# Kernel optimization log

Hardware: AMD Instinct MI355X
Metric: run time of the kernel (lower is better)

## Reference

```python
import jax, jax.numpy as jnp
import numpy as np

B, N, D, L = 8, 2048, 256, 4
LN_EPS = 1e-5


def setup_inputs() -> dict:
    key = jax.random.key(0)
    ks = jax.random.split(key, 12)
    s = 1.0 / np.sqrt(D)  # keep relu-attention scores well-scaled
    return {
        "x": jax.random.normal(ks[0], (B, N, D), jnp.float32),
        "wpe": jax.random.normal(ks[1], (N, D), jnp.float32) * 0.02,
        "Wq": jax.random.normal(ks[2], (L, D, D), jnp.float32) * s,
        "Wk": jax.random.normal(ks[3], (L, D, D), jnp.float32) * s,
        "Wv": jax.random.normal(ks[4], (L, D, D), jnp.float32) * s,
        "ln1_g": jnp.ones((L, D), jnp.float32),
        "ln1_b": jnp.zeros((L, D), jnp.float32),
        "mlp_W1": jax.random.normal(ks[5], (L, D, D), jnp.float32) * s,
        "mlp_b1": jnp.zeros((L, D), jnp.float32),
        "mlp_W2": jax.random.normal(ks[6], (L, D, D), jnp.float32) * s,
        "mlp_b2": jnp.zeros((L, D), jnp.float32),
        "ln2_g": jnp.ones((L, D), jnp.float32),
        "ln2_b": jnp.zeros((L, D), jnp.float32),
    }


def _layernorm(h, g, b):
    mu = jnp.mean(h, axis=-1, keepdims=True)
    var = jnp.mean(jnp.square(h - mu), axis=-1, keepdims=True)
    return (h - mu) * jax.lax.rsqrt(var + LN_EPS) * g + b


def reference(x, wpe, Wq, Wk, Wv, ln1_g, ln1_b, mlp_W1, mlp_b1, mlp_W2, mlp_b2, ln2_g, ln2_b):
    n = x.shape[1]
    # causal averaging mask: mask[i,j] = 1/(i+1) if j <= i else 0
    idx = jnp.arange(n)
    mask = (idx[None, :] <= idx[:, None]).astype(x.dtype) / (idx[:, None] + 1).astype(x.dtype)
    H = x + wpe[:n][None, :, :]  # positional embedding (position_ids = arange)
    for l in range(L):
        q = jnp.einsum('bnd,de->bne', H, Wq[l])
        k = jnp.einsum('bnd,de->bne', H, Wk[l])
        v = jnp.einsum('bnd,de->bne', H, Wv[l])
        attn = jax.nn.relu(jnp.einsum('bid,bjd->bij', q, k)) * mask[None, :, :]
        H = H + jnp.einsum('bij,bjd->bid', attn, v)
        H = _layernorm(H, ln1_g[l], ln1_b[l])
        h1 = jax.nn.relu(jnp.einsum('bnd,de->bne', H, mlp_W1[l]) + mlp_b1[l])
        H = H + jnp.einsum('bnd,de->bne', h1, mlp_W2[l]) + mlp_b2[l]
        H = _layernorm(H, ln2_g[l], ln2_b[l])
    return H
```

## Files before the change

kernel.cpp:

```cpp
#include <hip/hip_runtime.h>

#define Dd 256
#define Nn 2048
#define Bb 8
#define Ll 4
#define Mm (Bb*Nn)

typedef __attribute__((ext_vector_type(8))) short short8;
typedef __attribute__((ext_vector_type(4))) float f32x4;
typedef unsigned short u16;

__device__ __forceinline__ u16 f2bf(float f) {
  unsigned int u = __float_as_uint(f);
  u = (u + 0x7FFFu + ((u >> 16) & 1u)) >> 16;
  return (u16)u;
}
__device__ __forceinline__ float bf2f(u16 h) {
  return __uint_as_float(((unsigned int)h) << 16);
}
__device__ __forceinline__ void split2(float v, u16& hi, u16& lo) {
  hi = f2bf(v);
  lo = f2bf(v - bf2f(hi));
}

__global__ void prep_w3(const float* __restrict__ Wq, const float* __restrict__ Wk,
                        const float* __restrict__ Wv, const float* __restrict__ W1,
                        const float* __restrict__ W2,
                        u16* __restrict__ qh, u16* __restrict__ ql,
                        u16* __restrict__ kh, u16* __restrict__ kl,
                        u16* __restrict__ vh, u16* __restrict__ vl,
                        u16* __restrict__ w1h, u16* __restrict__ w1l,
                        u16* __restrict__ w2h, u16* __restrict__ w2l) {
  int idx = blockIdx.x * 256 + threadIdx.x;
  int l = idx >> 16, rem = idx & 65535;
  int e = rem >> 8, d = rem & 255;
  int src = (l << 16) | (d << 8) | e;
  u16 h, lo;
  split2(Wq[src], h, lo); qh[idx] = h;  ql[idx] = lo;
  split2(Wk[src], h, lo); kh[idx] = h;  kl[idx] = lo;
  split2(Wv[src], h, lo); vh[idx] = h;  vl[idx] = lo;
  split2(W1[src], h, lo); w1h[idx] = h; w1l[idx] = lo;
  split2(W2[src], h, lo); w2h[idx] = h; w2l[idx] = lo;
}

__global__ void add_pe3(const float* __restrict__ x, const float* __restrict__ wpe,
                        float* __restrict__ H, u16* __restrict__ Hh, u16* __restrict__ Hl) {
  int idx = blockIdx.x * 256 + threadIdx.x;
  int nd = (idx << 2) & (Nn * Dd - 1);
  float4 xv = ((const float4*)x)[idx];
  float4 pv = *(const float4*)(wpe + nd);
  float4 h;
  h.x = xv.x + pv.x; h.y = xv.y + pv.y; h.z = xv.z + pv.z; h.w = xv.w + pv.w;
  ((float4*)H)[idx] = h;
  ushort4 hv, lv;
  split2(h.x, hv.x, lv.x); split2(h.y, hv.y, lv.y);
  split2(h.z, hv.z, lv.z); split2(h.w, hv.w, lv.w);
  ((ushort4*)Hh)[idx] = hv;
  ((ushort4*)Hl)[idx] = lv;
}

__global__ __launch_bounds__(256) void ln3(const float* __restrict__ Hin,
      float* __restrict__ Hout, u16* __restrict__ Hh, u16* __restrict__ Hl,
      const float* __restrict__ g, const float* __restrict__ b) {
  int w = threadIdx.x >> 6, l = threadIdx.x & 63;
  int row = blockIdx.x * 4 + w;
  const float4 h = *(const float4*)(Hin + row * Dd + l * 4);
  float s = h.x + h.y + h.z + h.w;
  #pragma unroll
  for (int m = 1; m < 64; m <<= 1) s += __shfl_xor(s, m, 64);
  float mu = s * (1.0f / Dd);
  float4 c; c.x = h.x - mu; c.y = h.y - mu; c.z = h.z - mu; c.w = h.w - mu;
  float sq = c.x*c.x + c.y*c.y + c.z*c.z + c.w*c.w;
  #pragma unroll
  for (int m = 1; m < 64; m <<= 1) sq += __shfl_xor(sq, m, 64);
  float rs = rsqrtf(sq * (1.0f / Dd) + 1e-5f);
  float4 gv = *(const float4*)(g + l * 4);
  float4 bv = *(const float4*)(b + l * 4);
  float4 y;
  y.x = c.x * rs * gv.x + bv.x;
  y.y = c.y * rs * gv.y + bv.y;
  y.z = c.z * rs * gv.z + bv.z;
  y.w = c.w * rs * gv.w + bv.w;
  *(float4*)(Hout + row * Dd + l * 4) = y;
  ushort4 hv, lv;
  split2(y.x, hv.x, lv.x); split2(y.y, hv.y, lv.y);
  split2(y.z, hv.z, lv.z); split2(y.w, hv.w, lv.w);
  *(ushort4*)(Hh + row * Dd + l * 4) = hv;
  *(ushort4*)(Hl + row * Dd + l * 4) = lv;
}

template<int EPI>
__global__ __launch_bounds__(256) void gemm3(
    const u16* __restrict__ Ah, const u16* __restrict__ Al,
    const u16* __restrict__ Bh, const u16* __restrict__ Bl,
    void* __restrict__ Ch, void* __restrict__ Cl, const float* __restrict__ bias,
    int ldc, long sBz, long sCz) {
  __shared__ u16 Sa[2][64 * 40];
  __shared__ u16 Sb[2][64 * 40];
  const int t = threadIdx.x;
  const int l = t & 63, w = t >> 6;
  const int m0 = blockIdx.x * 64, n0 = blockIdx.y * 64;
  Bh += (long)blockIdx.z * sBz;
  Bl += (long)blockIdx.z * sBz;
  const int lr = l & 15, lk = l >> 4;
  const int sr = t >> 2, sc = t & 3;

  const f32x4 zv = {0.f, 0.f, 0.f, 0.f};
  f32x4 acc[4];
  #pragma unroll
  for (int i = 0; i < 4; ++i) acc[i] = zv;

  for (int kt = 0; kt < 8; ++kt) {
    const int k0 = kt * 32;
    *(uint4*)(&Sa[0][sr * 40 + sc * 8]) = *(const uint4*)(Ah + (long)(m0 + sr) * 256 + k0 + sc * 8);
    *(uint4*)(&Sa[1][sr * 40 + sc * 8]) = *(const uint4*)(Al + (long)(m0 + sr) * 256 + k0 + sc * 8);
    *(uint4*)(&Sb[0][sr * 40 + sc * 8]) = *(const uint4*)(Bh + (long)(n0 + sr) * 256 + k0 + sc * 8);
    *(uint4*)(&Sb[1][sr * 40 + sc * 8]) = *(const uint4*)(Bl + (long)(n0 + sr) * 256 + k0 + sc * 8);
    __syncthreads();
    short8 ah = *(const short8*)(&Sa[0][(w * 16 + lr) * 40 + lk * 8]);
    short8 al = *(const short8*)(&Sa[1][(w * 16 + lr) * 40 + lk * 8]);
    short8 bh[4], bl[4];
    #pragma unroll
    for (int ni = 0; ni < 4; ++ni) {
      bh[ni] = *(const short8*)(&Sb[0][(ni * 16 + lr) * 40 + lk * 8]);
      bl[ni] = *(const short8*)(&Sb[1][(ni * 16 + lr) * 40 + lk * 8]);
    }
    #pragma unroll
    for (int ni = 0; ni < 4; ++ni) {
      acc[ni] = __builtin_amdgcn_mfma_f32_16x16x32_bf16(ah, bh[ni], acc[ni], 0, 0, 0);
      acc[ni] = __builtin_amdgcn_mfma_f32_16x16x32_bf16(ah, bl[ni], acc[ni], 0, 0, 0);
      acc[ni] = __builtin_amdgcn_mfma_f32_16x16x32_bf16(al, bh[ni], acc[ni], 0, 0, 0);
    }
    __syncthreads();
  }

  #pragma unroll
  for (int ni = 0; ni < 4; ++ni) {
    const int row = m0 + w * 16 + lk * 4;
    const int col = n0 + ni * 16 + lr;
    if constexpr (EPI == 0) {
      u16* Chb = (u16*)Ch + (long)blockIdx.z * sCz;
      u16* Clb = (u16*)Cl + (long)blockIdx.z * sCz;
      #pragma unroll
      for (int r = 0; r < 4; ++r) {
        u16 hi, lo; split2(acc[ni][r], hi, lo);
        Chb[(long)(row + r) * ldc + col] = hi;
        Clb[(long)(row + r) * ldc + col] = lo;
      }
    } else if constexpr (EPI == 1) {
      u16* Chb = (u16*)Ch;
      u16* Clb = (u16*)Cl;
      const float bi = bias[col];
      #pragma unroll
      for (int r = 0; r < 4; ++r) {
        float v = fmaxf(acc[ni][r] + bi, 0.0f);
        u16 hi, lo; split2(v, hi, lo);
        Chb[(long)(row + r) * ldc + col] = hi;
        Clb[(long)(row + r) * ldc + col] = lo;
      }
    } else if constexpr (EPI == 2) {
      float* Cf = (float*)Ch;
      const float bi = bias[col];
      #pragma unroll
      for (int r = 0; r < 4; ++r)
        Cf[(long)(row + r) * ldc + col] += acc[ni][r] + bi;
    } else {
      u16* Chb = (u16*)Ch + (long)blockIdx.z * sCz;
      u16* Clb = (u16*)Cl + (long)blockIdx.z * sCz;
      const long pbase = (long)(col >> 5) * (Dd * 32) + (col & 31);
      #pragma unroll
      for (int r = 0; r < 4; ++r) {
        u16 hi, lo; split2(acc[ni][r], hi, lo);
        Chb[pbase + (long)(row + r) * 32] = hi;
        Clb[pbase + (long)(row + r) * 32] = lo;
      }
    }
  }
}

__global__ __launch_bounds__(256) void attn4(
    const u16* __restrict__ Qh, const u16* __restrict__ Ql,
    const u16* __restrict__ Kh, const u16* __restrict__ Kl,
    const u16* __restrict__ Vph, const u16* __restrict__ Vpl,
    float* __restrict__ H) {
  __shared__ u16 Ksh[2][32 * 256];
  __shared__ u16 Vsh[2][256 * 32];
  __shared__ u16 P[4][2][16 * 56];
  const int t = threadIdx.x, l = t & 63, w = t >> 6;
  const int bx = blockIdx.x;
  const int b = bx & 7;
  const int c = (bx >> 3) & 7;
  const int qt = bx >> 6;
  const int kbeg = c * 256;
  if (kbeg > qt * 64 + 63) return;
  const int q0 = qt * 64 + w * 16;
  const int kend_blk = min(kbeg + 256, qt * 64 + 64);
  const int lr = l & 15, lk = l >> 4;

  const u16* Qhp = Qh + (long)(b * Nn + q0 + lr) * Dd;
  const u16* Qlp = Ql + (long)(b * Nn + q0 + lr) * Dd;
  short8 qhf[8], qlf[8];
  #pragma unroll
  for (int cc = 0; cc < 8; ++cc) {
    qhf[cc] = *(const short8*)(Qhp + cc * 32 + lk * 8);
    qlf[cc] = *(const short8*)(Qlp + cc * 32 + lk * 8);
  }

  const f32x4 zv = {0.f, 0.f, 0.f, 0.f};
  f32x4 o[16];
  #pragma unroll
  for (int i = 0; i < 16; ++i) o[i] = zv;

  u16* Ph = &P[w][0][0];
  u16* Pl = &P[w][1][0];
  const u16* Khb = Kh + (long)b * Nn * Dd;
  const u16* Klb = Kl + (long)b * Nn * Dd;
  const u16* Vphb = Vph + (long)b * Dd * Nn;
  const u16* Vplb = Vpl + (long)b * Dd * Nn;
  char* Kc0 = (char*)&Ksh[0][0];
  char* Kc1 = (char*)&Ksh[1][0];
  char* Vc0 = (char*)&Vsh[0][0];
  char* Vc1 = (char*)&Vsh[1][0];
  const int xr = (lr & 7) << 4;
  const int sr = t >> 3, sc8 = t & 7;

  for (int k0 = kbeg; k0 < kend_blk; k0 += 32) {
    {
      const long krow = (long)(k0 + sr) * Dd + sc8 * 32;
      const u16* vph = Vphb + (long)(k0 >> 5) * (Dd * 32) + t * 32;
      const u16* vpl = Vplb + (long)(k0 >> 5) * (Dd * 32) + t * 32;
      uint4 ka[4], kb[4], va[4], vb[4];
      #pragma unroll
      for (int i = 0; i < 4; ++i) {
        ka[i] = *(const uint4*)(Khb + krow + i * 8);
        kb[i] = *(const uint4*)(Klb + krow + i * 8);
        va[i] = *(const uint4*)(vph + i * 8);
        vb[i] = *(const uint4*)(vpl + i * 8);
      }
      #pragma unroll
      for (int i = 0; i < 4; ++i) {
        const int ko = (sr * 512 + sc8 * 64 + i * 16) ^ ((sr & 7) << 4);
        const int vo = (t * 64 + i * 16) ^ ((t & 7) << 4);
        *(uint4*)(Kc0 + ko) = ka[i];
        *(uint4*)(Kc1 + ko) = kb[i];
        *(uint4*)(Vc0 + vo) = va[i];
        *(uint4*)(Vc1 + vo) = vb[i];
      }
    }
    __syncthreads();

    if (k0 <= q0 + 15) {
      f32x4 s0 = zv, s1 = zv;
      #pragma unroll
      for (int cc = 0; cc < 8; ++cc) {
        const int ko = (lr * 512 + cc * 64 + lk * 16) ^ xr;
        short8 kh0 = *(const short8*)(Kc0 + ko);
        short8 kl0 = *(const short8*)(Kc1 + ko);
        short8 kh1 = *(const short8*)(Kc0 + ko + 8192);
        short8 kl1 = *(const short8*)(Kc1 + ko + 8192);
        s0 = __builtin_amdgcn_mfma_f32_16x16x32_bf16(qhf[cc], kh0, s0, 0, 0, 0);
        s0 = __builtin_amdgcn_mfma_f32_16x16x32_bf16(qhf[cc], kl0, s0, 0, 0, 0);
        s0 = __builtin_amdgcn_mfma_f32_16x16x32_bf16(qlf[cc], kh0, s0, 0, 0, 0);
        s1 = __builtin_amdgcn_mfma_f32_16x16x32_bf16(qhf[cc], kh1, s1, 0, 0, 0);
        s1 = __builtin_amdgcn_mfma_f32_16x16x32_bf16(qhf[cc], kl1, s1, 0, 0, 0);
        s1 = __builtin_amdgcn_mfma_f32_16x16x32_bf16(qlf[cc], kh1, s1, 0, 0, 0);
      }
      #pragma unroll
      for (int r = 0; r < 4; ++r) {
        const int i = q0 + lk * 4 + r;
        {
          const int j = k0 + lr;
          float v = s0[r];
          v = (j <= i && v > 0.0f) ? v : 0.0f;
          u16 hi, lo; split2(v, hi, lo);
          Ph[(lk * 4 + r) * 56 + lr] = hi;
          Pl[(lk * 4 + r) * 56 + lr] = lo;
        }
        {
          const int j = k0 + 16 + lr;
          float v = s1[r];
          v = (j <= i && v > 0.0f) ? v : 0.0f;
          u16 hi, lo; split2(v, hi, lo);
          Ph[(lk * 4 + r) * 56 + 16 + lr] = hi;
          Pl[(lk * 4 + r) * 56 + 16 + lr] = lo;
        }
      }
      short8 pfh = *(const short8*)(Ph + lr * 56 + lk * 8);
      short8 pfl = *(const short8*)(Pl + lr * 56 + lk * 8);
      #pragma unroll
      for (int dt = 0; dt < 16; ++dt) {
        const int vo = ((dt * 16 + lr) * 64 + lk * 16) ^ xr;
        short8 vh = *(const short8*)(Vc0 + vo);
        short8 vl = *(const short8*)(Vc1 + vo);
        o[dt] = __builtin_amdgcn_mfma_f32_16x16x32_bf16(pfh, vh, o[dt], 0, 0, 0);
        o[dt] = __builtin_amdgcn_mfma_f32_16x16x32_bf16(pfh, vl, o[dt], 0, 0, 0);
        o[dt] = __builtin_amdgcn_mfma_f32_16x16x32_bf16(pfl, vh, o[dt], 0, 0, 0);
      }
    }
    __syncthreads();
  }

  if (kbeg <= q0 + 15) {
    #pragma unroll
    for (int r = 0; r < 4; ++r) {
      const int i = q0 + lk * 4 + r;
      const float sc = 1.0f / (float)(i + 1);
      float* Hp = H + (long)(b * Nn + i) * Dd;
      #pragma unroll
      for (int dt = 0; dt < 16; ++dt)
        atomicAdd(Hp + dt * 16 + lr, o[dt][r] * sc);
    }
  }
}

extern "C" void kernel_launch(void* const* d_in, const int* in_sizes, int n_in,
                              void* d_out, int out_size, void* d_ws, size_t ws_size,
                              hipStream_t stream) {
  const float* x    = (const float*)d_in[0];
  const float* wpe  = (const float*)d_in[1];
  const float* Wq   = (const float*)d_in[2];
  const float* Wk   = (const float*)d_in[3];
  const float* Wv   = (const float*)d_in[4];
  const float* ln1g = (const float*)d_in[5];
  const float* ln1b = (const float*)d_in[6];
  const float* W1   = (const float*)d_in[7];
  const float* b1   = (const float*)d_in[8];
  const float* W2   = (const float*)d_in[9];
  const float* b2   = (const float*)d_in[10];
  const float* ln2g = (const float*)d_in[11];
  const float* ln2b = (const float*)d_in[12];

  char* p = (char*)d_ws;
  auto alloc = [&](size_t bytes) -> void* {
    void* r = (void*)p;
    p += (bytes + 255) & ~(size_t)255;
    return r;
  };
  float* H = (float*)alloc((size_t)Mm * Dd * 4);
  u16* Hh  = (u16*)alloc((size_t)Mm * Dd * 2);
  u16* Hl  = (u16*)alloc((size_t)Mm * Dd * 2);
  u16* Qh_ = (u16*)alloc((size_t)Mm * Dd * 2);
  u16* Ql_ = (u16*)alloc((size_t)Mm * Dd * 2);
  u16* Kh_ = (u16*)alloc((size_t)Mm * Dd * 2);
  u16* Kl_ = (u16*)alloc((size_t)Mm * Dd * 2);
  u16* Vh_ = (u16*)alloc((size_t)Mm * Dd * 2);
  u16* Vl_ = (u16*)alloc((size_t)Mm * Dd * 2);
  const size_t wsz = (size_t)Ll * Dd * Dd * 2;
  u16* Wqh = (u16*)alloc(wsz); u16* Wql = (u16*)alloc(wsz);
  u16* Wkh = (u16*)alloc(wsz); u16* Wkl = (u16*)alloc(wsz);
  u16* Wvh = (u16*)alloc(wsz); u16* Wvl = (u16*)alloc(wsz);
  u16* W1h = (u16*)alloc(wsz); u16* W1l = (u16*)alloc(wsz);
  u16* W2h = (u16*)alloc(wsz); u16* W2l = (u16*)alloc(wsz);

  prep_w3<<<1024, 256, 0, stream>>>(Wq, Wk, Wv, W1, W2,
      Wqh, Wql, Wkh, Wkl, Wvh, Wvl, W1h, W1l, W2h, W2l);
  add_pe3<<<Mm * Dd / 4 / 256, 256, 0, stream>>>(x, wpe, H, Hh, Hl);

  const dim3 g1(Mm / 64, Dd / 64, 1);
  const dim3 gv(Dd / 64, Nn / 64, Bb);
  const long NDl = (long)Nn * Dd;

  for (int l = 0; l < Ll; ++l) {
    const int wo = l * Dd * Dd;
    gemm3<0><<<g1, 256, 0, stream>>>(Hh, Hl, Wqh + wo, Wql + wo, Qh_, Ql_, nullptr, Dd, 0, 0);
    gemm3<0><<<g1, 256, 0, stream>>>(Hh, Hl, Wkh + wo, Wkl + wo, Kh_, Kl_, nullptr, Dd, 0, 0);
    gemm3<3><<<gv, 256, 0, stream>>>(Wvh + wo, Wvl + wo, Hh, Hl, Vh_, Vl_, nullptr, Nn, NDl, NDl);
    attn4<<<2048, 256, 0, stream>>>(Qh_, Ql_, Kh_, Kl_, Vh_, Vl_, H);
    ln3<<<Mm / 4, 256, 0, stream>>>(H, H, Hh, Hl, ln1g + l * Dd, ln1b + l * Dd);
    gemm3<1><<<g1, 256, 0, stream>>>(Hh, Hl, W1h + wo, W1l + wo, Qh_, Ql_, b1 + l * Dd, Dd, 0, 0);
    gemm3<2><<<g1, 256, 0, stream>>>(Qh_, Ql_, W2h + wo, W2l + wo, (void*)H, nullptr, b2 + l * Dd, Dd, 0, 0);
    float* lnout = (l == Ll - 1) ? (float*)d_out : H;
    ln3<<<Mm / 4, 256, 0, stream>>>(H, lnout, Hh, Hl, ln2g + l * Dd, ln2b + l * Dd);
  }
}
```

Measured before the change: 1.163 ms.

## Compact attention grid heaviest-first, prefetch next K/V tile into registers, raise MFMA priority

The attention grid is remapped so only causally live (query tile, key chunk) blocks launch (1152 instead of 2048), ordered from the longest query tiles down to balance load. Global loads for the next K/V tile are issued right after the shared-memory store and barrier, so they overlap with the current tile's MFMA work. The K staging thread mapping changes and s_setprio brackets the MFMA loops to favour matrix issue. The risks are extra register pressure from the held prefetch buffers and a small serial loop per block to decode its index.

```diff
diff --git a/kernel.cpp b/kernel.cpp
--- a/kernel.cpp
+++ b/kernel.cpp
@@ -178,7 +178,7 @@
   }
 }
 
-__global__ __launch_bounds__(256) void attn4(
+__global__ __launch_bounds__(256) void attn7(
     const u16* __restrict__ Qh, const u16* __restrict__ Ql,
     const u16* __restrict__ Kh, const u16* __restrict__ Kl,
     const u16* __restrict__ Vph, const u16* __restrict__ Vpl,
@@ -187,12 +187,13 @@
   __shared__ u16 Vsh[2][256 * 32];
   __shared__ u16 P[4][2][16 * 56];
   const int t = threadIdx.x, l = t & 63, w = t >> 6;
-  const int bx = blockIdx.x;
-  const int b = bx & 7;
-  const int c = (bx >> 3) & 7;
-  const int qt = bx >> 6;
+  const int b = blockIdx.x & 7;
+  const int pidx = blockIdx.x >> 3;
+  int g = 0, acc_ = 0;
+  while (acc_ + (8 - (g >> 2)) <= pidx) { acc_ += 8 - (g >> 2); ++g; }
+  const int qt = 31 - g;
+  const int c = pidx - acc_;
   const int kbeg = c * 256;
-  if (kbeg > qt * 64 + 63) return;
   const int q0 = qt * 64 + w * 16;
   const int kend_blk = min(kbeg + 256, qt * 64 + 64);
   const int lr = l & 15, lk = l >> 4;
@@ -222,14 +223,37 @@
   char* Vc0 = (char*)&Vsh[0][0];
   char* Vc1 = (char*)&Vsh[1][0];
   const int xr = (lr & 7) << 4;
-  const int sr = t >> 3, sc8 = t & 7;
+  const int ksr = t & 31, ksc = t >> 5;
+
+  uint4 ka[4], kb[4], va[4], vb[4];
+  {
+    const long krow = (long)(kbeg + ksr) * Dd + ksc * 32;
+    const u16* vph = Vphb + (long)(kbeg >> 5) * (Dd * 32) + t * 32;
+    const u16* vpl = Vplb + (long)(kbeg >> 5) * (Dd * 32) + t * 32;
+    #pragma unroll
+    for (int i = 0; i < 4; ++i) {
+      ka[i] = *(const uint4*)(Khb + krow + i * 8);
+      kb[i] = *(const uint4*)(Klb + krow + i * 8);
+      va[i] = *(const uint4*)(vph + i * 8);
+      vb[i] = *(const uint4*)(vpl + i * 8);
+    }
+  }
 
   for (int k0 = kbeg; k0 < kend_blk; k0 += 32) {
-    {
-      const long krow = (long)(k0 + sr) * Dd + sc8 * 32;
-      const u16* vph = Vphb + (long)(k0 >> 5) * (Dd * 32) + t * 32;
-      const u16* vpl = Vplb + (long)(k0 >> 5) * (Dd * 32) + t * 32;
-      uint4 ka[4], kb[4], va[4], vb[4];
+    #pragma unroll
+    for (int i = 0; i < 4; ++i) {
+      const int ko = (ksr * 512 + ksc * 64 + i * 16) ^ ((ksr & 7) << 4);
+      const int vo = (t * 64 + i * 16) ^ ((t & 7) << 4);
+      *(uint4*)(Kc0 + ko) = ka[i];
+      *(uint4*)(Kc1 + ko) = kb[i];
+      *(uint4*)(Vc0 + vo) = va[i];
+      *(uint4*)(Vc1 + vo) = vb[i];
+    }
+    __syncthreads();
+    if (k0 + 32 < kend_blk) {
+      const long krow = (long)(k0 + 32 + ksr) * Dd + ksc * 32;
+      const u16* vph = Vphb + (long)((k0 + 32) >> 5) * (Dd * 32) + t * 32;
+      const u16* vpl = Vplb + (long)((k0 + 32) >> 5) * (Dd * 32) + t * 32;
       #pragma unroll
       for (int i = 0; i < 4; ++i) {
         ka[i] = *(const uint4*)(Khb + krow + i * 8);
@@ -237,20 +261,11 @@
         va[i] = *(const uint4*)(vph + i * 8);
         vb[i] = *(const uint4*)(vpl + i * 8);
       }
-      #pragma unroll
-      for (int i = 0; i < 4; ++i) {
-        const int ko = (sr * 512 + sc8 * 64 + i * 16) ^ ((sr & 7) << 4);
-        const int vo = (t * 64 + i * 16) ^ ((t & 7) << 4);
-        *(uint4*)(Kc0 + ko) = ka[i];
-        *(uint4*)(Kc1 + ko) = kb[i];
-        *(uint4*)(Vc0 + vo) = va[i];
-        *(uint4*)(Vc1 + vo) = vb[i];
-      }
-    }
-    __syncthreads();
+    }
 
     if (k0 <= q0 + 15) {
       f32x4 s0 = zv, s1 = zv;
+      __builtin_amdgcn_s_setprio(1);
       #pragma unroll
       for (int cc = 0; cc < 8; ++cc) {
         const int ko = (lr * 512 + cc * 64 + lk * 16) ^ xr;
@@ -265,6 +280,7 @@
         s1 = __builtin_amdgcn_mfma_f32_16x16x32_bf16(qhf[cc], kl1, s1, 0, 0, 0);
         s1 = __builtin_amdgcn_mfma_f32_16x16x32_bf16(qlf[cc], kh1, s1, 0, 0, 0);
       }
+      __builtin_amdgcn_s_setprio(0);
       #pragma unroll
       for (int r = 0; r < 4; ++r) {
         const int i = q0 + lk * 4 + r;
@@ -287,6 +303,7 @@
       }
       short8 pfh = *(const short8*)(Ph + lr * 56 + lk * 8);
       short8 pfl = *(const short8*)(Pl + lr * 56 + lk * 8);
+      __builtin_amdgcn_s_setprio(1);
       #pragma unroll
       for (int dt = 0; dt < 16; ++dt) {
         const int vo = ((dt * 16 + lr) * 64 + lk * 16) ^ xr;
@@ -296,20 +313,19 @@
         o[dt] = __builtin_amdgcn_mfma_f32_16x16x32_bf16(pfh, vl, o[dt], 0, 0, 0);
         o[dt] = __builtin_amdgcn_mfma_f32_16x16x32_bf16(pfl, vh, o[dt], 0, 0, 0);
       }
+      __builtin_amdgcn_s_setprio(0);
     }
     __syncthreads();
   }
 
-  if (kbeg <= q0 + 15) {
-    #pragma unroll
-    for (int r = 0; r < 4; ++r) {
-      const int i = q0 + lk * 4 + r;
-      const float sc = 1.0f / (float)(i + 1);
-      float* Hp = H + (long)(b * Nn + i) * Dd;
-      #pragma unroll
-      for (int dt = 0; dt < 16; ++dt)
-        atomicAdd(Hp + dt * 16 + lr, o[dt][r] * sc);
-    }
+  #pragma unroll
+  for (int r = 0; r < 4; ++r) {
+    const int i = q0 + lk * 4 + r;
+    const float sc = 1.0f / (float)(i + 1);
+    float* Hp = H + (long)(b * Nn + i) * Dd;
+    #pragma unroll
+    for (int dt = 0; dt < 16; ++dt)
+      atomicAdd(Hp + dt * 16 + lr, o[dt][r] * sc);
   }
 }
 
@@ -365,7 +381,7 @@
     gemm3<0><<<g1, 256, 0, stream>>>(Hh, Hl, Wqh + wo, Wql + wo, Qh_, Ql_, nullptr, Dd, 0, 0);
     gemm3<0><<<g1, 256, 0, stream>>>(Hh, Hl, Wkh + wo, Wkl + wo, Kh_, Kl_, nullptr, Dd, 0, 0);
     gemm3<3><<<gv, 256, 0, stream>>>(Wvh + wo, Wvl + wo, Hh, Hl, Vh_, Vl_, nullptr, Nn, NDl, NDl);
-    attn4<<<2048, 256, 0, stream>>>(Qh_, Ql_, Kh_, Kl_, Vh_, Vl_, H);
+    attn7<<<1152, 256, 0, stream>>>(Qh_, Ql_, Kh_, Kl_, Vh_, Vl_, H);
     ln3<<<Mm / 4, 256, 0, stream>>>(H, H, Hh, Hl, ln1g + l * Dd, ln1b + l * Dd);
     gemm3<1><<<g1, 256, 0, stream>>>(Hh, Hl, W1h + wo, W1l + wo, Qh_, Ql_, b1 + l * Dd, Dd, 0, 0);
     gemm3<2><<<g1, 256, 0, stream>>>(Qh_, Ql_, W2h + wo, W2l + wo, (void*)H, nullptr, b2 + l * Dd, Dd, 0, 0);
```

After: 1.752 ms. +50.7%, slower.

## Enlarge GEMM M-tile to 128 rows and restage attention K/V loads with chunk swizzle

Applied to the files above, without the earlier changes.

The split-bf16 GEMM now computes a 128x64 tile per block, with each wave holding two 16-row A fragments, so every B fragment loaded from LDS is reused twice and the grid halves. The attention kernel changes how K and V tiles are staged into shared memory: lanes now read contiguous 16-byte chunks of each K row, and the XOR swizzle is applied at chunk granularity, with the reads updated to match. This aims to improve global-load coalescing and reduce LDS bank conflicts, at the cost of more accumulator registers in the GEMM and fewer blocks for tail balance.

```diff
diff --git a/kernel.cpp b/kernel.cpp
--- a/kernel.cpp
+++ b/kernel.cpp
@@ -90,95 +90,108 @@
 }
 
 template<int EPI>
-__global__ __launch_bounds__(256) void gemm3(
+__global__ __launch_bounds__(256) void gemm4(
     const u16* __restrict__ Ah, const u16* __restrict__ Al,
     const u16* __restrict__ Bh, const u16* __restrict__ Bl,
     void* __restrict__ Ch, void* __restrict__ Cl, const float* __restrict__ bias,
     int ldc, long sBz, long sCz) {
-  __shared__ u16 Sa[2][64 * 40];
+  __shared__ u16 Sa[2][128 * 40];
   __shared__ u16 Sb[2][64 * 40];
   const int t = threadIdx.x;
   const int l = t & 63, w = t >> 6;
-  const int m0 = blockIdx.x * 64, n0 = blockIdx.y * 64;
+  const int m0 = blockIdx.x * 128, n0 = blockIdx.y * 64;
   Bh += (long)blockIdx.z * sBz;
   Bl += (long)blockIdx.z * sBz;
   const int lr = l & 15, lk = l >> 4;
-  const int sr = t >> 2, sc = t & 3;
+  const int ar = t >> 1, ac = (t & 1) << 1;
+  const int br = t >> 2, bc = t & 3;
 
   const f32x4 zv = {0.f, 0.f, 0.f, 0.f};
-  f32x4 acc[4];
-  #pragma unroll
-  for (int i = 0; i < 4; ++i) acc[i] = zv;
+  f32x4 acc[2][4];
+  #pragma unroll
+  for (int i = 0; i < 2; ++i)
+    #pragma unroll
+    for (int j = 0; j < 4; ++j) acc[i][j] = zv;
 
   for (int kt = 0; kt < 8; ++kt) {
     const int k0 = kt * 32;
-    *(uint4*)(&Sa[0][sr * 40 + sc * 8]) = *(const uint4*)(Ah + (long)(m0 + sr) * 256 + k0 + sc * 8);
-    *(uint4*)(&Sa[1][sr * 40 + sc * 8]) = *(const uint4*)(Al + (long)(m0 + sr) * 256 + k0 + sc * 8);
-    *(uint4*)(&Sb[0][sr * 40 + sc * 8]) = *(const uint4*)(Bh + (long)(n0 + sr) * 256 + k0 + sc * 8);
-    *(uint4*)(&Sb[1][sr * 40 + sc * 8]) = *(const uint4*)(Bl + (long)(n0 + sr) * 256 + k0 + sc * 8);
+    *(uint4*)(&Sa[0][ar * 40 + ac * 8])     = *(const uint4*)(Ah + (long)(m0 + ar) * 256 + k0 + ac * 8);
+    *(uint4*)(&Sa[0][ar * 40 + ac * 8 + 8]) = *(const uint4*)(Ah + (long)(m0 + ar) * 256 + k0 + ac * 8 + 8);
+    *(uint4*)(&Sa[1][ar * 40 + ac * 8])     = *(const uint4*)(Al + (long)(m0 + ar) * 256 + k0 + ac * 8);
+    *(uint4*)(&Sa[1][ar * 40 + ac * 8 + 8]) = *(const uint4*)(Al + (long)(m0 + ar) * 256 + k0 + ac * 8 + 8);
+    *(uint4*)(&Sb[0][br * 40 + bc * 8])     = *(const uint4*)(Bh + (long)(n0 + br) * 256 + k0 + bc * 8);
+    *(uint4*)(&Sb[1][br * 40 + bc * 8])     = *(const uint4*)(Bl + (long)(n0 + br) * 256 + k0 + bc * 8);
     __syncthreads();
-    short8 ah = *(const short8*)(&Sa[0][(w * 16 + lr) * 40 + lk * 8]);
-    short8 al = *(const short8*)(&Sa[1][(w * 16 + lr) * 40 + lk * 8]);
-    short8 bh[4], bl[4];
+    short8 ah[2], al[2], bh[4], bl[4];
+    #pragma unroll
+    for (int mi = 0; mi < 2; ++mi) {
+      ah[mi] = *(const short8*)(&Sa[0][(w * 32 + mi * 16 + lr) * 40 + lk * 8]);
+      al[mi] = *(const short8*)(&Sa[1][(w * 32 + mi * 16 + lr) * 40 + lk * 8]);
+    }
     #pragma unroll
     for (int ni = 0; ni < 4; ++ni) {
       bh[ni] = *(const short8*)(&Sb[0][(ni * 16 + lr) * 40 + lk * 8]);
       bl[ni] = *(const short8*)(&Sb[1][(ni * 16 + lr) * 40 + lk * 8]);
     }
     #pragma unroll
+    for (int mi = 0; mi < 2; ++mi)
+      #pragma unroll
+      for (int ni = 0; ni < 4; ++ni) {
+        acc[mi][ni] = __builtin_amdgcn_mfma_f32_16x16x32_bf16(ah[mi], bh[ni], acc[mi][ni], 0, 0, 0);
+        acc[mi][ni] = __builtin_amdgcn_mfma_f32_16x16x32_bf16(ah[mi], bl[ni], acc[mi][ni], 0, 0, 0);
+        acc[mi][ni] = __builtin_amdgcn_mfma_f32_16x16x32_bf16(al[mi], bh[ni], acc[mi][ni], 0, 0, 0);
+      }
+    __syncthreads();
+  }
+
+  #pragma unroll
+  for (int mi = 0; mi < 2; ++mi) {
+    #pragma unroll
     for (int ni = 0; ni < 4; ++ni) {
-      acc[ni] = __builtin_amdgcn_mfma_f32_16x16x32_bf16(ah, bh[ni], acc[ni], 0, 0, 0);
-      acc[ni] = __builtin_amdgcn_mfma_f32_16x16x32_bf16(ah, bl[ni], acc[ni], 0, 0, 0);
-      acc[ni] = __builtin_amdgcn_mfma_f32_16x16x32_bf16(al, bh[ni], acc[ni], 0, 0, 0);
-    }
-    __syncthreads();
-  }
-
-  #pragma unroll
-  for (int ni = 0; ni < 4; ++ni) {
-    const int row = m0 + w * 16 + lk * 4;
-    const int col = n0 + ni * 16 + lr;
-    if constexpr (EPI == 0) {
-      u16* Chb = (u16*)Ch + (long)blockIdx.z * sCz;
-      u16* Clb = (u16*)Cl + (long)blockIdx.z * sCz;
-      #pragma unroll
-      for (int r = 0; r < 4; ++r) {
-        u16 hi, lo; split2(acc[ni][r], hi, lo);
-        Chb[(long)(row + r) * ldc + col] = hi;
-        Clb[(long)(row + r) * ldc + col] = lo;
-      }
-    } else if constexpr (EPI == 1) {
-      u16* Chb = (u16*)Ch;
-      u16* Clb = (u16*)Cl;
-      const float bi = bias[col];
-      #pragma unroll
-      for (int r = 0; r < 4; ++r) {
-        float v = fmaxf(acc[ni][r] + bi, 0.0f);
-        u16 hi, lo; split2(v, hi, lo);
-        Chb[(long)(row + r) * ldc + col] = hi;
-        Clb[(long)(row + r) * ldc + col] = lo;
-      }
-    } else if constexpr (EPI == 2) {
-      float* Cf = (float*)Ch;
-      const float bi = bias[col];
-      #pragma unroll
-      for (int r = 0; r < 4; ++r)
-        Cf[(long)(row + r) * ldc + col] += acc[ni][r] + bi;
-    } else {
-      u16* Chb = (u16*)Ch + (long)blockIdx.z * sCz;
-      u16* Clb = (u16*)Cl + (long)blockIdx.z * sCz;
-      const long pbase = (long)(col >> 5) * (Dd * 32) + (col & 31);
-      #pragma unroll
-      for (int r = 0; r < 4; ++r) {
-        u16 hi, lo; split2(acc[ni][r], hi, lo);
-        Chb[pbase + (long)(row + r) * 32] = hi;
-        Clb[pbase + (long)(row + r) * 32] = lo;
-      }
-    }
-  }
-}
-
-__global__ __launch_bounds__(256) void attn4(
+      const int row = m0 + w * 32 + mi * 16 + lk * 4;
+      const int col = n0 + ni * 16 + lr;
+      if constexpr (EPI == 0) {
+        u16* Chb = (u16*)Ch + (long)blockIdx.z * sCz;
+        u16* Clb = (u16*)Cl + (long)blockIdx.z * sCz;
+        #pragma unroll
+        for (int r = 0; r < 4; ++r) {
+          u16 hi, lo; split2(acc[mi][ni][r], hi, lo);
+          Chb[(long)(row + r) * ldc + col] = hi;
+          Clb[(long)(row + r) * ldc + col] = lo;
+        }
+      } else if constexpr (EPI == 1) {
+        u16* Chb = (u16*)Ch;
+        u16* Clb = (u16*)Cl;
+        const float bi = bias[col];
+        #pragma unroll
+        for (int r = 0; r < 4; ++r) {
+          float v = fmaxf(acc[mi][ni][r] + bi, 0.0f);
+          u16 hi, lo; split2(v, hi, lo);
+          Chb[(long)(row + r) * ldc + col] = hi;
+          Clb[(long)(row + r) * ldc + col] = lo;
+        }
+      } else if constexpr (EPI == 2) {
+        float* Cf = (float*)Ch;
+        const float bi = bias[col];
+        #pragma unroll
+        for (int r = 0; r < 4; ++r)
+          Cf[(long)(row + r) * ldc + col] += acc[mi][ni][r] + bi;
+      } else {
+        u16* Chb = (u16*)Ch + (long)blockIdx.z * sCz;
+        u16* Clb = (u16*)Cl + (long)blockIdx.z * sCz;
+        const long pbase = (long)(col >> 5) * (Dd * 32) + (col & 31);
+        #pragma unroll
+        for (int r = 0; r < 4; ++r) {
+          u16 hi, lo; split2(acc[mi][ni][r], hi, lo);
+          Chb[pbase + (long)(row + r) * 32] = hi;
+          Clb[pbase + (long)(row + r) * 32] = lo;
+        }
+      }
+    }
+  }
+}
+
+__global__ __launch_bounds__(256) void attn8(
     const u16* __restrict__ Qh, const u16* __restrict__ Ql,
     const u16* __restrict__ Kh, const u16* __restrict__ Kl,
     const u16* __restrict__ Vph, const u16* __restrict__ Vpl,
@@ -221,30 +234,30 @@
   char* Kc1 = (char*)&Ksh[1][0];
   char* Vc0 = (char*)&Vsh[0][0];
   char* Vc1 = (char*)&Vsh[1][0];
-  const int xr = (lr & 7) << 4;
-  const int sr = t >> 3, sc8 = t & 7;
+  const int kr = (w << 3) + (l >> 3);
+  const int kc = l & 7;
+  const int krx = (l >> 3) << 2;
 
   for (int k0 = kbeg; k0 < kend_blk; k0 += 32) {
     {
-      const long krow = (long)(k0 + sr) * Dd + sc8 * 32;
-      const u16* vph = Vphb + (long)(k0 >> 5) * (Dd * 32) + t * 32;
-      const u16* vpl = Vplb + (long)(k0 >> 5) * (Dd * 32) + t * 32;
-      uint4 ka[4], kb[4], va[4], vb[4];
+      const u16* krp0 = Khb + (long)(k0 + kr) * Dd;
+      const u16* krp1 = Klb + (long)(k0 + kr) * Dd;
+      const u16* vpp0 = Vphb + (long)(k0 >> 5) * (Dd * 32);
+      const u16* vpp1 = Vplb + (long)(k0 >> 5) * (Dd * 32);
       #pragma unroll
       for (int i = 0; i < 4; ++i) {
-        ka[i] = *(const uint4*)(Khb + krow + i * 8);
-        kb[i] = *(const uint4*)(Klb + krow + i * 8);
-        va[i] = *(const uint4*)(vph + i * 8);
-        vb[i] = *(const uint4*)(vpl + i * 8);
-      }
-      #pragma unroll
-      for (int i = 0; i < 4; ++i) {
-        const int ko = (sr * 512 + sc8 * 64 + i * 16) ^ ((sr & 7) << 4);
-        const int vo = (t * 64 + i * 16) ^ ((t & 7) << 4);
-        *(uint4*)(Kc0 + ko) = ka[i];
-        *(uint4*)(Kc1 + ko) = kb[i];
-        *(uint4*)(Vc0 + vo) = va[i];
-        *(uint4*)(Vc1 + vo) = vb[i];
+        const int kchunk = i * 8 + kc;
+        const int ko = kr * 512 + ((kchunk ^ krx) << 4);
+        uint4 ka = *(const uint4*)(krp0 + kchunk * 8);
+        uint4 kb = *(const uint4*)(krp1 + kchunk * 8);
+        *(uint4*)(Kc0 + ko) = ka;
+        *(uint4*)(Kc1 + ko) = kb;
+        const int vd = i * 64 + (t >> 2);
+        const int vo = vd * 64 + (((t & 3) ^ (vd & 3)) << 4);
+        uint4 va = *(const uint4*)(vpp0 + (long)vd * 32 + (t & 3) * 8);
+        uint4 vb = *(const uint4*)(vpp1 + (long)vd * 32 + (t & 3) * 8);
+        *(uint4*)(Vc0 + vo) = va;
+        *(uint4*)(Vc1 + vo) = vb;
       }
     }
     __syncthreads();
@@ -253,7 +266,7 @@
       f32x4 s0 = zv, s1 = zv;
       #pragma unroll
       for (int cc = 0; cc < 8; ++cc) {
-        const int ko = (lr * 512 + cc * 64 + lk * 16) ^ xr;
+        const int ko = lr * 512 + ((((cc << 2) + lk) ^ ((lr & 7) << 2)) << 4);
         short8 kh0 = *(const short8*)(Kc0 + ko);
         short8 kl0 = *(const short8*)(Kc1 + ko);
         short8 kh1 = *(const short8*)(Kc0 + ko + 8192);
@@ -289,7 +302,7 @@
       short8 pfl = *(const short8*)(Pl + lr * 56 + lk * 8);
       #pragma unroll
       for (int dt = 0; dt < 16; ++dt) {
-        const int vo = ((dt * 16 + lr) * 64 + lk * 16) ^ xr;
+        const int vo = (dt * 16 + lr) * 64 + ((lk ^ (lr & 3)) << 4);
         short8 vh = *(const short8*)(Vc0 + vo);
         short8 vl = *(const short8*)(Vc1 + vo);
         o[dt] = __builtin_amdgcn_mfma_f32_16x16x32_bf16(pfh, vh, o[dt], 0, 0, 0);
@@ -356,19 +369,19 @@
       Wqh, Wql, Wkh, Wkl, Wvh, Wvl, W1h, W1l, W2h, W2l);
   add_pe3<<<Mm * Dd / 4 / 256, 256, 0, stream>>>(x, wpe, H, Hh, Hl);
 
-  const dim3 g1(Mm / 64, Dd / 64, 1);
-  const dim3 gv(Dd / 64, Nn / 64, Bb);
+  const dim3 g1(Mm / 128, Dd / 64, 1);
+  const dim3 gv(Dd / 128, Nn / 64, Bb);
   const long NDl = (long)Nn * Dd;
 
   for (int l = 0; l < Ll; ++l) {
     const int wo = l * Dd * Dd;
-    gemm3<0><<<g1, 256, 0, stream>>>(Hh, Hl, Wqh + wo, Wql + wo, Qh_, Ql_, nullptr, Dd, 0, 0);
-    gemm3<0><<<g1, 256, 0, stream>>>(Hh, Hl, Wkh + wo, Wkl + wo, Kh_, Kl_, nullptr, Dd, 0, 0);
-    gemm3<3><<<gv, 256, 0, stream>>>(Wvh + wo, Wvl + wo, Hh, Hl, Vh_, Vl_, nullptr, Nn, NDl, NDl);
-    attn4<<<2048, 256, 0, stream>>>(Qh_, Ql_, Kh_, Kl_, Vh_, Vl_, H);
+    gemm4<0><<<g1, 256, 0, stream>>>(Hh, Hl, Wqh + wo, Wql + wo, Qh_, Ql_, nullptr, Dd, 0, 0);
+    gemm4<0><<<g1, 256, 0, stream>>>(Hh, Hl, Wkh + wo, Wkl + wo, Kh_, Kl_, nullptr, Dd, 0, 0);
+    gemm4<3><<<gv, 256, 0, stream>>>(Wvh + wo, Wvl + wo, Hh, Hl, Vh_, Vl_, nullptr, Nn, NDl, NDl);
+    attn8<<<2048, 256, 0, stream>>>(Qh_, Ql_, Kh_, Kl_, Vh_, Vl_, H);
     ln3<<<Mm / 4, 256, 0, stream>>>(H, H, Hh, Hl, ln1g + l * Dd, ln1b + l * Dd);
-    gemm3<1><<<g1, 256, 0, stream>>>(Hh, Hl, W1h + wo, W1l + wo, Qh_, Ql_, b1 + l * Dd, Dd, 0, 0);
-    gemm3<2><<<g1, 256, 0, stream>>>(Qh_, Ql_, W2h + wo, W2l + wo, (void*)H, nullptr, b2 + l * Dd, Dd, 0, 0);
+    gemm4<1><<<g1, 256, 0, stream>>>(Hh, Hl, W1h + wo, W1l + wo, Qh_, Ql_, b1 + l * Dd, Dd, 0, 0);
+    gemm4<2><<<g1, 256, 0, stream>>>(Qh_, Ql_, W2h + wo, W2l + wo, (void*)H, nullptr, b2 + l * Dd, Dd, 0, 0);
     float* lnout = (l == Ll - 1) ? (float*)d_out : H;
     ln3<<<Mm / 4, 256, 0, stream>>>(H, lnout, Hh, Hl, ln2g + l * Dd, ln2b + l * Dd);
   }
```

New measurement: 979.1 us. 15.8% less time.
